# Performance work log

Hardware: AMD Instinct MI355X
Metric: run time of the kernel (lower is better)

Reference implementation:

```python
import jax, jax.numpy as jnp
import numpy as np

QUERY_DIM = 768
KEY_DIM = 1024


def setup_inputs() -> dict:
    key = jax.random.key(0)
    ks = jax.random.split(key, 8)
    B, LQ, LK = 16, 2048, 2048
    s_q = 1.0 / np.sqrt(QUERY_DIM)
    s_k = 1.0 / np.sqrt(KEY_DIM)
    return {
        "query": jax.random.normal(ks[0], (B, LQ, QUERY_DIM), jnp.float32),
        "key": jax.random.normal(ks[1], (B, LK, KEY_DIM), jnp.float32),
        "Wq": jax.random.uniform(ks[2], (QUERY_DIM, KEY_DIM), jnp.float32, -s_q, s_q),
        "bq": jax.random.uniform(ks[3], (KEY_DIM,), jnp.float32, -s_q, s_q),
        "Wk": jax.random.uniform(ks[4], (KEY_DIM, KEY_DIM), jnp.float32, -s_k, s_k),
        "bk": jax.random.uniform(ks[5], (KEY_DIM,), jnp.float32, -s_k, s_k),
        "Wv": jax.random.uniform(ks[6], (KEY_DIM, KEY_DIM), jnp.float32, -s_k, s_k),
        "bv": jax.random.uniform(ks[7], (KEY_DIM,), jnp.float32, -s_k, s_k),
    }


def reference(query, key, Wq, bq, Wk, bk, Wv, bv):
    # Linear projections (single-head)
    q = jnp.einsum('bqd,dk->bqk', query, Wq) + bq  # [B, Lq, Dk]
    k = jnp.einsum('bsd,dk->bsk', key, Wk) + bk    # [B, Lk, Dk]
    v = jnp.einsum('bsd,dk->bsk', key, Wv) + bv    # [B, Lk, Dk]
    d_k = k.shape[-1]
    scores = jnp.einsum('bqk,bsk->bqs', q, k) / jnp.sqrt(jnp.asarray(d_k, q.dtype))
    weights = jax.nn.softmax(scores, axis=-1)      # [B, Lq, Lk]
    return jnp.einsum('bqs,bsk->bqk', weights, v)  # [B, Lq, Dk]
```

## Files before the change

kernel.cpp:

```cpp
#include <hip/hip_runtime.h>
#include <hip/hip_bf16.h>


typedef __attribute__((ext_vector_type(4))) float  f32x4;
typedef __attribute__((ext_vector_type(8))) __bf16 bf16x8;

#define BM 128
#define BN 128
#define BK 64

__device__ __forceinline__ void gload_lds16(const __bf16* g, __bf16* l) {
    __builtin_amdgcn_global_load_lds(
        (const __attribute__((address_space(1))) void*)g,
        (__attribute__((address_space(3))) void*)l, 16, 0, 0);
}

enum { MODE_PROJ = 0, MODE_PROJT = 1, MODE_SCORE = 2, MODE_PV = 3 };

__device__ __forceinline__ int lds_off(int R, int kc) {
    return R * BK + ((kc ^ (R & 7)) * 8);
}

template <int MODE>
__global__ __launch_bounds__(256) void gemm128(
    const __bf16* __restrict__ Ag, const __bf16* __restrict__ Bg,
    const float* __restrict__ aux,
    float* __restrict__ rs,
    void* __restrict__ Cg,
    int K, int lda, int ldb, int ldc,
    long batchA, long batchB, long batchC, long batchRS)
{
    __shared__ __bf16 As[BM * BK];
    __shared__ __bf16 Bs[BN * BK];
    const int t    = threadIdx.x;
    const int lane = t & 63;
    const int w    = t >> 6;
    const int quad = lane >> 4;
    const int l15  = lane & 15;
    const int wm   = w >> 1, wn = w & 1;
    const int m0   = blockIdx.x * BM;
    const int n0   = blockIdx.y * BN;
    const int z    = blockIdx.z;

    const __bf16* A = Ag + (long)z * batchA;
    const __bf16* B = Bg + (long)z * batchB;

    const int srow = lane >> 3;
    const int kcs  = ((lane & 7) ^ srow) * 8;

    const __bf16* ap[4];
    const __bf16* bp[4];
    #pragma unroll
    for (int i = 0; i < 4; ++i) {
        const int seg = w * 4 + i;
        ap[i] = A + (long)(m0 + seg * 8 + srow) * lda + kcs;
        bp[i] = B + (long)(n0 + seg * 8 + srow) * ldb + kcs;
    }

    f32x4 acc[4][4];
    #pragma unroll
    for (int jm = 0; jm < 4; ++jm)
        #pragma unroll
        for (int jn = 0; jn < 4; ++jn) acc[jm][jn] = (f32x4)(0.0f);

    for (int k0 = 0; k0 < K; k0 += BK) {
        #pragma unroll
        for (int i = 0; i < 4; ++i) {
            const int seg = w * 4 + i;
            gload_lds16(ap[i], As + seg * 512);
            gload_lds16(bp[i], Bs + seg * 512);
            ap[i] += BK;
            bp[i] += BK;
        }
        __syncthreads();
        #pragma unroll
        for (int kh = 0; kh < 2; ++kh) {
            bf16x8 af[4], bfr[4];
            #pragma unroll
            for (int j = 0; j < 4; ++j) {
                const int Ra = wm * 64 + j * 16 + l15;
                const int Rb = wn * 64 + j * 16 + l15;
                const int kc = kh * 4 + quad;
                af[j]  = *(const bf16x8*)&As[lds_off(Ra, kc)];
                bfr[j] = *(const bf16x8*)&Bs[lds_off(Rb, kc)];
            }
            #pragma unroll
            for (int jm = 0; jm < 4; ++jm)
                #pragma unroll
                for (int jn = 0; jn < 4; ++jn)
                    acc[jm][jn] = __builtin_amdgcn_mfma_f32_16x16x32_bf16(
                        af[jm], bfr[jn], acc[jm][jn], 0, 0, 0);
        }
        __syncthreads();
    }

    const int rowbase = m0 + wm * 64;
    const int colbase = n0 + wn * 64;

    if constexpr (MODE == MODE_PROJ) {
        __bf16* C = (__bf16*)Cg;
        #pragma unroll
        for (int jn = 0; jn < 4; ++jn) {
            const int col = colbase + jn * 16 + l15;
            const float bv = aux[col];
            #pragma unroll
            for (int jm = 0; jm < 4; ++jm)
                #pragma unroll
                for (int r = 0; r < 4; ++r) {
                    const int row = rowbase + jm * 16 + quad * 4 + r;
                    C[(long)row * ldc + col] = (__bf16)(acc[jm][jn][r] + bv);
                }
        }
    } else if constexpr (MODE == MODE_PROJT) {
        __bf16* C = (__bf16*)Cg;
        #pragma unroll
        for (int jm = 0; jm < 4; ++jm)
            #pragma unroll
            for (int r = 0; r < 4; ++r) {
                const int row = rowbase + jm * 16 + quad * 4 + r;
                const float bv = aux[row];
                #pragma unroll
                for (int jn = 0; jn < 4; ++jn) {
                    const int col = colbase + jn * 16 + l15;
                    const long idx = (long)(col >> 11) * (1024L * 2048)
                                   + (long)row * 2048 + (col & 2047);
                    C[idx] = (__bf16)(acc[jm][jn][r] + bv);
                }
            }
    } else if constexpr (MODE == MODE_SCORE) {
        const float sc = 0.03125f * 1.44269504088896f;
        __bf16* C = (__bf16*)Cg + (long)z * batchC;
        float* rsz = rs + (long)z * batchRS;
        #pragma unroll
        for (int jm = 0; jm < 4; ++jm) {
            float s[4] = {0.f, 0.f, 0.f, 0.f};
            #pragma unroll
            for (int jn = 0; jn < 4; ++jn) {
                const int col = colbase + jn * 16 + l15;
                #pragma unroll
                for (int r = 0; r < 4; ++r) {
                    const int row = rowbase + jm * 16 + quad * 4 + r;
                    const float e = exp2f(acc[jm][jn][r] * sc);
                    C[(long)row * ldc + col] = (__bf16)e;
                    s[r] += e;
                }
            }
            #pragma unroll
            for (int r = 0; r < 4; ++r) {
                float v = s[r];
                v += __shfl_xor(v, 1);
                v += __shfl_xor(v, 2);
                v += __shfl_xor(v, 4);
                v += __shfl_xor(v, 8);
                if (l15 == 0)
                    atomicAdd(&rsz[rowbase + jm * 16 + quad * 4 + r], v);
            }
        }
    } else {
        float* C = (float*)Cg + (long)z * batchC;
        const float* rsz = rs + (long)z * batchRS;
        #pragma unroll
        for (int jm = 0; jm < 4; ++jm) {
            float inv[4];
            #pragma unroll
            for (int r = 0; r < 4; ++r)
                inv[r] = 1.0f / rsz[rowbase + jm * 16 + quad * 4 + r];
            #pragma unroll
            for (int jn = 0; jn < 4; ++jn) {
                const int col = colbase + jn * 16 + l15;
                #pragma unroll
                for (int r = 0; r < 4; ++r) {
                    const int row = rowbase + jm * 16 + quad * 4 + r;
                    C[(long)row * ldc + col] = acc[jm][jn][r] * inv[r];
                }
            }
        }
    }
}

__global__ __launch_bounds__(256) void conv_bf16(const float* __restrict__ in,
                                                 __bf16* __restrict__ out, long n8)
{
    const long stride = (long)gridDim.x * blockDim.x;
    for (long i = (long)blockIdx.x * blockDim.x + threadIdx.x; i < n8; i += stride) {
        const float4* p = (const float4*)(in + i * 8);
        const float4 a = p[0], b = p[1];
        bf16x8 o;
        o[0] = (__bf16)a.x; o[1] = (__bf16)a.y; o[2] = (__bf16)a.z; o[3] = (__bf16)a.w;
        o[4] = (__bf16)b.x; o[5] = (__bf16)b.y; o[6] = (__bf16)b.z; o[7] = (__bf16)b.w;
        *(bf16x8*)(out + i * 8) = o;
    }
}

__global__ __launch_bounds__(256) void transpose_w(const float* __restrict__ W,
                                                   __bf16* __restrict__ WT,
                                                   int K, int N)
{
    __shared__ float tile[32][33];
    const int n0 = blockIdx.x * 32, k0 = blockIdx.y * 32;
    const int c = threadIdx.x & 31, r4 = threadIdx.x >> 5;
    #pragma unroll
    for (int i = 0; i < 4; ++i) {
        const int r = r4 + i * 8;
        tile[r][c] = W[(long)(k0 + r) * N + n0 + c];
    }
    __syncthreads();
    #pragma unroll
    for (int i = 0; i < 4; ++i) {
        const int r = r4 + i * 8;
        WT[(long)(n0 + r) * K + k0 + c] = (__bf16)tile[c][r];
    }
}

extern "C" void kernel_launch(void* const* d_in, const int* in_sizes, int n_in,
                              void* d_out, int out_size, void* d_ws, size_t ws_size,
                              hipStream_t stream) {
    const float* query = (const float*)d_in[0];
    const float* key   = (const float*)d_in[1];
    const float* Wq    = (const float*)d_in[2];
    const float* bq    = (const float*)d_in[3];
    const float* Wk    = (const float*)d_in[4];
    const float* bk    = (const float*)d_in[5];
    const float* Wv    = (const float*)d_in[6];
    const float* bv    = (const float*)d_in[7];
    float* out = (float*)d_out;

    const int B = 16, Lq = 2048, Lk = 2048, Dq = 768, Dk = 1024;
    const long M = (long)B * Lq;

    char* base = (char*)d_ws;
    __bf16* P   = (__bf16*)base;
    __bf16* qa  = (__bf16*)base;
    __bf16* ka  = (__bf16*)(base + 50331648);
    __bf16* WqT = (__bf16*)(base + 117440512);
    __bf16* WkT = (__bf16*)(base + 119013376);
    __bf16* WvT = (__bf16*)(base + 121110528);
    char* p2 = base + 134217728;
    __bf16* q  = (__bf16*)p2;  p2 += M * Dk * 2;
    __bf16* k  = (__bf16*)p2;  p2 += M * Dk * 2;
    __bf16* vT = (__bf16*)p2;  p2 += M * Dk * 2;
    float* row_sum = (float*)p2; p2 += M * 4;
    if ((size_t)(p2 - base) > ws_size) return;

    dim3 blk(256);

    conv_bf16<<<512, blk, 0, stream>>>(query, qa, M * Dq / 8);
    conv_bf16<<<512, blk, 0, stream>>>(key,   ka, M * Dk / 8);
    transpose_w<<<dim3(Dk / 32, Dq / 32), blk, 0, stream>>>(Wq, WqT, Dq, Dk);
    transpose_w<<<dim3(Dk / 32, Dk / 32), blk, 0, stream>>>(Wk, WkT, Dk, Dk);
    transpose_w<<<dim3(Dk / 32, Dk / 32), blk, 0, stream>>>(Wv, WvT, Dk, Dk);
    hipMemsetAsync(row_sum, 0, M * 4, stream);

    gemm128<MODE_PROJ><<<dim3(M / BM, Dk / BN, 1), blk, 0, stream>>>(
        qa, WqT, bq, nullptr, q, Dq, Dq, Dq, Dk, 0, 0, 0, 0);
    gemm128<MODE_PROJ><<<dim3(M / BM, Dk / BN, 1), blk, 0, stream>>>(
        ka, WkT, bk, nullptr, k, Dk, Dk, Dk, Dk, 0, 0, 0, 0);
    gemm128<MODE_PROJT><<<dim3(Dk / BM, M / BN, 1), blk, 0, stream>>>(
        WvT, ka, bv, nullptr, vT, Dk, Dk, Dk, 0, 0, 0, 0, 0);

    gemm128<MODE_SCORE><<<dim3(Lq / BM, Lk / BN, B), blk, 0, stream>>>(
        q, k, nullptr, row_sum, P, Dk, Dk, Dk, Lk,
        (long)Lq * Dk, (long)Lk * Dk, (long)Lq * Lk, Lq);

    gemm128<MODE_PV><<<dim3(Lq / BM, Dk / BN, B), blk, 0, stream>>>(
        P, vT, nullptr, row_sum, out, Lk, Lk, 2048, Dk,
        (long)Lq * Lk, 1024L * 2048, (long)Lq * Dk, Lq);
}
```

Measured before the change: 1.006 ms.

## Switch GEMMs to 256x256 tiles with 4-stage LDS pipeline and 8 waves

Replaces the 128x128x64 single-buffered GEMM with a 256x256x32 kernel using 512 threads and a 4-deep LDS ring fed by async global-to-LDS loads. Loads for future tiles are issued while MFMAs run, with explicit vmcnt waits, barriers and s_setprio around the compute phases. This targets load latency and the per-iteration sync stalls, and larger tiles raise data reuse. In exchange it needs more registers and LDS (64KB), which may limit occupancy, and the hand-tuned waitcnt/barrier schedule is fragile.

```diff
diff --git a/kernel.cpp b/kernel.cpp
--- a/kernel.cpp
+++ b/kernel.cpp
@@ -5,9 +5,9 @@
 typedef __attribute__((ext_vector_type(4))) float  f32x4;
 typedef __attribute__((ext_vector_type(8))) __bf16 bf16x8;
 
-#define BM 128
-#define BN 128
-#define BK 64
+#define BM 256
+#define BN 256
+#define BK 32
 
 __device__ __forceinline__ void gload_lds16(const __bf16* g, __bf16* l) {
     __builtin_amdgcn_global_load_lds(
@@ -17,12 +17,61 @@
 
 enum { MODE_PROJ = 0, MODE_PROJT = 1, MODE_SCORE = 2, MODE_PV = 3 };
 
-__device__ __forceinline__ int lds_off(int R, int kc) {
-    return R * BK + ((kc ^ (R & 7)) * 8);
-}
+#define MF(m_, a_)                                                              \
+    acc[m_][0] = __builtin_amdgcn_mfma_f32_16x16x32_bf16(a_, b0, acc[m_][0], 0, 0, 0); \
+    acc[m_][1] = __builtin_amdgcn_mfma_f32_16x16x32_bf16(a_, b1, acc[m_][1], 0, 0, 0); \
+    acc[m_][2] = __builtin_amdgcn_mfma_f32_16x16x32_bf16(a_, b2, acc[m_][2], 0, 0, 0); \
+    acc[m_][3] = __builtin_amdgcn_mfma_f32_16x16x32_bf16(a_, b3, acc[m_][3], 0, 0, 0);
+
+#define TILE_STEP(B_, NB_, DO_STAGE, VM_WAIT) do {                              \
+    const __bf16* __restrict__ Ab = As[B_];                                     \
+    const __bf16* __restrict__ Bb = Bs[B_];                                     \
+    bf16x8 a0, a1, a2, a3, a4, a5, a6, a7, b0, b1, b2, b3;                      \
+                                        \
+    a0 = *(const bf16x8*)&Ab[raA];                                              \
+    a1 = *(const bf16x8*)&Ab[raA + 512];                                        \
+    a2 = *(const bf16x8*)&Ab[raA + 1024];                                       \
+    a3 = *(const bf16x8*)&Ab[raA + 1536];                                       \
+    b0 = *(const bf16x8*)&Bb[raB];                                              \
+    b1 = *(const bf16x8*)&Bb[raB + 512];                                        \
+    b2 = *(const bf16x8*)&Bb[raB + 1024];                                       \
+    b3 = *(const bf16x8*)&Bb[raB + 1536];                                       \
+    if (DO_STAGE) {                                                             \
+        gload_lds16(ap0, &As[NB_][wA]);                                         \
+        gload_lds16(ap1, &As[NB_][wA + 512]);                                   \
+        ap0 += BK; ap1 += BK;                                                   \
+    }                                                                           \
+    asm volatile("" ::: "memory");                                              \
+    __builtin_amdgcn_s_barrier();                                               \
+    asm volatile("s_waitcnt lgkmcnt(0)" ::: "memory");                          \
+    __builtin_amdgcn_s_setprio(1);                                              \
+    MF(0, a0) MF(1, a1) MF(2, a2) MF(3, a3)                                     \
+    __builtin_amdgcn_s_setprio(0);                                              \
+    asm volatile("" ::: "memory");                                              \
+    __builtin_amdgcn_s_barrier();                                               \
+                        \
+    a4 = *(const bf16x8*)&Ab[raA + 2048];                                       \
+    a5 = *(const bf16x8*)&Ab[raA + 2560];                                       \
+    a6 = *(const bf16x8*)&Ab[raA + 3072];                                       \
+    a7 = *(const bf16x8*)&Ab[raA + 3584];                                       \
+    if (DO_STAGE) {                                                             \
+        gload_lds16(bp0, &Bs[NB_][wA]);                                         \
+        gload_lds16(bp1, &Bs[NB_][wA + 512]);                                   \
+        bp0 += BK; bp1 += BK;                                                   \
+    }                                                                           \
+    VM_WAIT;                                                                    \
+    asm volatile("" ::: "memory");                                              \
+    __builtin_amdgcn_s_barrier();                                               \
+    asm volatile("s_waitcnt lgkmcnt(0)" ::: "memory");                          \
+    __builtin_amdgcn_s_setprio(1);                                              \
+    MF(4, a4) MF(5, a5) MF(6, a6) MF(7, a7)                                     \
+    __builtin_amdgcn_s_setprio(0);                                              \
+    asm volatile("" ::: "memory");                                              \
+    __builtin_amdgcn_s_barrier();                                               \
+} while (0)
 
 template <int MODE>
-__global__ __launch_bounds__(256) void gemm128(
+__global__ __launch_bounds__(512, 2) void gemm256(
     const __bf16* __restrict__ Ag, const __bf16* __restrict__ Bg,
     const float* __restrict__ aux,
     float* __restrict__ rs,
@@ -30,14 +79,14 @@
     int K, int lda, int ldb, int ldc,
     long batchA, long batchB, long batchC, long batchRS)
 {
-    __shared__ __bf16 As[BM * BK];
-    __shared__ __bf16 Bs[BN * BK];
+    __shared__ __bf16 As[4][BM * BK];
+    __shared__ __bf16 Bs[4][BN * BK];
     const int t    = threadIdx.x;
     const int lane = t & 63;
     const int w    = t >> 6;
     const int quad = lane >> 4;
     const int l15  = lane & 15;
-    const int wm   = w >> 1, wn = w & 1;
+    const int wm   = w >> 2, wn = w & 3;
     const int m0   = blockIdx.x * BM;
     const int n0   = blockIdx.y * BN;
     const int z    = blockIdx.z;
@@ -45,86 +94,76 @@
     const __bf16* A = Ag + (long)z * batchA;
     const __bf16* B = Bg + (long)z * batchB;
 
-    const int srow = lane >> 3;
-    const int kcs  = ((lane & 7) ^ srow) * 8;
-
-    const __bf16* ap[4];
-    const __bf16* bp[4];
+    const int srow = lane >> 2;
+    const int sq   = ((lane & 3) ^ ((lane >> 3) & 3)) * 8;
+    const __bf16* ap0 = A + (long)(m0 + w * 32 +      srow) * lda + sq;
+    const __bf16* ap1 = A + (long)(m0 + w * 32 + 16 + srow) * lda + sq;
+    const __bf16* bp0 = B + (long)(n0 + w * 32 +      srow) * ldb + sq;
+    const __bf16* bp1 = B + (long)(n0 + w * 32 + 16 + srow) * ldb + sq;
+    const int wA = w * 1024;
+
+    const int swz = (quad ^ ((l15 >> 1) & 3)) * 8;
+    const int raA = (wm * 128 + l15) * BK + swz;
+    const int raB = (wn * 64  + l15) * BK + swz;
+
+    f32x4 acc[8][4];
     #pragma unroll
-    for (int i = 0; i < 4; ++i) {
-        const int seg = w * 4 + i;
-        ap[i] = A + (long)(m0 + seg * 8 + srow) * lda + kcs;
-        bp[i] = B + (long)(n0 + seg * 8 + srow) * ldb + kcs;
-    }
-
-    f32x4 acc[4][4];
+    for (int i = 0; i < 8; ++i)
+        #pragma unroll
+        for (int j = 0; j < 4; ++j) acc[i][j] = (f32x4)(0.0f);
+
+    const int NT = K / BK;
+
     #pragma unroll
-    for (int jm = 0; jm < 4; ++jm)
-        #pragma unroll
-        for (int jn = 0; jn < 4; ++jn) acc[jm][jn] = (f32x4)(0.0f);
-
-    for (int k0 = 0; k0 < K; k0 += BK) {
-        #pragma unroll
-        for (int i = 0; i < 4; ++i) {
-            const int seg = w * 4 + i;
-            gload_lds16(ap[i], As + seg * 512);
-            gload_lds16(bp[i], Bs + seg * 512);
-            ap[i] += BK;
-            bp[i] += BK;
-        }
-        __syncthreads();
-        #pragma unroll
-        for (int kh = 0; kh < 2; ++kh) {
-            bf16x8 af[4], bfr[4];
-            #pragma unroll
-            for (int j = 0; j < 4; ++j) {
-                const int Ra = wm * 64 + j * 16 + l15;
-                const int Rb = wn * 64 + j * 16 + l15;
-                const int kc = kh * 4 + quad;
-                af[j]  = *(const bf16x8*)&As[lds_off(Ra, kc)];
-                bfr[j] = *(const bf16x8*)&Bs[lds_off(Rb, kc)];
-            }
-            #pragma unroll
-            for (int jm = 0; jm < 4; ++jm)
-                #pragma unroll
-                for (int jn = 0; jn < 4; ++jn)
-                    acc[jm][jn] = __builtin_amdgcn_mfma_f32_16x16x32_bf16(
-                        af[jm], bfr[jn], acc[jm][jn], 0, 0, 0);
-        }
-        __syncthreads();
-    }
-
-    const int rowbase = m0 + wm * 64;
+    for (int i = 0; i < 3; ++i) {
+        gload_lds16(ap0, &As[i][wA]);
+        gload_lds16(ap1, &As[i][wA + 512]);
+        gload_lds16(bp0, &Bs[i][wA]);
+        gload_lds16(bp1, &Bs[i][wA + 512]);
+        ap0 += BK; ap1 += BK; bp0 += BK; bp1 += BK;
+    }
+    asm volatile("s_waitcnt vmcnt(8)" ::: "memory");
+    __builtin_amdgcn_s_barrier();
+
+    for (int tt = 0; tt < NT - 3; ++tt) {
+        const int b = tt & 3, nb = (tt + 3) & 3;
+        TILE_STEP(b, nb, 1, asm volatile("s_waitcnt vmcnt(8)" ::: "memory"));
+    }
+    TILE_STEP((NT - 3) & 3, 0, 0, asm volatile("s_waitcnt vmcnt(4)" ::: "memory"));
+    TILE_STEP((NT - 2) & 3, 0, 0, asm volatile("s_waitcnt vmcnt(0)" ::: "memory"));
+    TILE_STEP((NT - 1) & 3, 0, 0, ((void)0));
+
+    const int rowbase = m0 + wm * 128;
     const int colbase = n0 + wn * 64;
 
     if constexpr (MODE == MODE_PROJ) {
         __bf16* C = (__bf16*)Cg;
         #pragma unroll
-        for (int jn = 0; jn < 4; ++jn) {
-            const int col = colbase + jn * 16 + l15;
+        for (int n = 0; n < 4; ++n) {
+            const int col = colbase + n * 16 + l15;
             const float bv = aux[col];
             #pragma unroll
-            for (int jm = 0; jm < 4; ++jm)
+            for (int m = 0; m < 8; ++m)
                 #pragma unroll
                 for (int r = 0; r < 4; ++r) {
-                    const int row = rowbase + jm * 16 + quad * 4 + r;
-                    C[(long)row * ldc + col] = (__bf16)(acc[jm][jn][r] + bv);
+                    const int row = rowbase + m * 16 + quad * 4 + r;
+                    C[(long)row * ldc + col] = (__bf16)(acc[m][n][r] + bv);
                 }
         }
     } else if constexpr (MODE == MODE_PROJT) {
         __bf16* C = (__bf16*)Cg;
         #pragma unroll
-        for (int jm = 0; jm < 4; ++jm)
+        for (int m = 0; m < 8; ++m)
             #pragma unroll
             for (int r = 0; r < 4; ++r) {
-                const int row = rowbase + jm * 16 + quad * 4 + r;
+                const int row = rowbase + m * 16 + quad * 4 + r;
                 const float bv = aux[row];
                 #pragma unroll
-                for (int jn = 0; jn < 4; ++jn) {
-                    const int col = colbase + jn * 16 + l15;
+                for (int n = 0; n < 4; ++n) {
+                    const int col = colbase + n * 16 + l15;
                     const long idx = (long)(col >> 11) * (1024L * 2048)
                                    + (long)row * 2048 + (col & 2047);
-                    C[idx] = (__bf16)(acc[jm][jn][r] + bv);
+                    C[idx] = (__bf16)(acc[m][n][r] + bv);
                 }
             }
     } else if constexpr (MODE == MODE_SCORE) {
@@ -132,15 +171,15 @@
         __bf16* C = (__bf16*)Cg + (long)z * batchC;
         float* rsz = rs + (long)z * batchRS;
         #pragma unroll
-        for (int jm = 0; jm < 4; ++jm) {
+        for (int m = 0; m < 8; ++m) {
             float s[4] = {0.f, 0.f, 0.f, 0.f};
             #pragma unroll
-            for (int jn = 0; jn < 4; ++jn) {
-                const int col = colbase + jn * 16 + l15;
+            for (int n = 0; n < 4; ++n) {
+                const int col = colbase + n * 16 + l15;
                 #pragma unroll
                 for (int r = 0; r < 4; ++r) {
-                    const int row = rowbase + jm * 16 + quad * 4 + r;
-                    const float e = exp2f(acc[jm][jn][r] * sc);
+                    const int row = rowbase + m * 16 + quad * 4 + r;
+                    const float e = exp2f(acc[m][n][r] * sc);
                     C[(long)row * ldc + col] = (__bf16)e;
                     s[r] += e;
                 }
@@ -153,25 +192,25 @@
                 v += __shfl_xor(v, 4);
                 v += __shfl_xor(v, 8);
                 if (l15 == 0)
-                    atomicAdd(&rsz[rowbase + jm * 16 + quad * 4 + r], v);
+                    atomicAdd(&rsz[rowbase + m * 16 + quad * 4 + r], v);
             }
         }
     } else {
         float* C = (float*)Cg + (long)z * batchC;
         const float* rsz = rs + (long)z * batchRS;
         #pragma unroll
-        for (int jm = 0; jm < 4; ++jm) {
+        for (int m = 0; m < 8; ++m) {
             float inv[4];
             #pragma unroll
             for (int r = 0; r < 4; ++r)
-                inv[r] = 1.0f / rsz[rowbase + jm * 16 + quad * 4 + r];
-            #pragma unroll
-            for (int jn = 0; jn < 4; ++jn) {
-                const int col = colbase + jn * 16 + l15;
+                inv[r] = 1.0f / rsz[rowbase + m * 16 + quad * 4 + r];
+            #pragma unroll
+            for (int n = 0; n < 4; ++n) {
+                const int col = colbase + n * 16 + l15;
                 #pragma unroll
                 for (int r = 0; r < 4; ++r) {
-                    const int row = rowbase + jm * 16 + quad * 4 + r;
-                    C[(long)row * ldc + col] = acc[jm][jn][r] * inv[r];
+                    const int row = rowbase + m * 16 + quad * 4 + r;
+                    C[(long)row * ldc + col] = acc[m][n][r] * inv[r];
                 }
             }
         }
@@ -243,6 +282,7 @@
     if ((size_t)(p2 - base) > ws_size) return;
 
     dim3 blk(256);
+    dim3 blk5(512);
 
     conv_bf16<<<512, blk, 0, stream>>>(query, qa, M * Dq / 8);
     conv_bf16<<<512, blk, 0, stream>>>(key,   ka, M * Dk / 8);
@@ -251,18 +291,18 @@
     transpose_w<<<dim3(Dk / 32, Dk / 32), blk, 0, stream>>>(Wv, WvT, Dk, Dk);
     hipMemsetAsync(row_sum, 0, M * 4, stream);
 
-    gemm128<MODE_PROJ><<<dim3(M / BM, Dk / BN, 1), blk, 0, stream>>>(
+    gemm256<MODE_PROJ><<<dim3(M / BM, Dk / BN, 1), blk5, 0, stream>>>(
         qa, WqT, bq, nullptr, q, Dq, Dq, Dq, Dk, 0, 0, 0, 0);
-    gemm128<MODE_PROJ><<<dim3(M / BM, Dk / BN, 1), blk, 0, stream>>>(
+    gemm256<MODE_PROJ><<<dim3(M / BM, Dk / BN, 1), blk5, 0, stream>>>(
         ka, WkT, bk, nullptr, k, Dk, Dk, Dk, Dk, 0, 0, 0, 0);
-    gemm128<MODE_PROJT><<<dim3(Dk / BM, M / BN, 1), blk, 0, stream>>>(
+    gemm256<MODE_PROJT><<<dim3(Dk / BM, M / BN, 1), blk5, 0, stream>>>(
         WvT, ka, bv, nullptr, vT, Dk, Dk, Dk, 0, 0, 0, 0, 0);
 
-    gemm128<MODE_SCORE><<<dim3(Lq / BM, Lk / BN, B), blk, 0, stream>>>(
+    gemm256<MODE_SCORE><<<dim3(Lq / BM, Lk / BN, B), blk5, 0, stream>>>(
         q, k, nullptr, row_sum, P, Dk, Dk, Dk, Lk,
         (long)Lq * Dk, (long)Lk * Dk, (long)Lq * Lk, Lq);
 
-    gemm128<MODE_PV><<<dim3(Lq / BM, Dk / BN, B), blk, 0, stream>>>(
+    gemm256<MODE_PV><<<dim3(Lq / BM, Dk / BN, B), blk5, 0, stream>>>(
         P, vT, nullptr, row_sum, out, Lk, Lk, 2048, Dk,
         (long)Lq * Lk, 1024L * 2048, (long)Lq * Dk, Lq);
 }
```

New measurement: 995.1 us. Within noise of the previous version (-1.0%).
